# Kernel tuning notes

Measured on AMD Instinct MI355X. Metric: run time of the kernel, lower is better.

## Reference

```python
import jax, jax.numpy as jnp
import numpy as np

N = 8192
DIMS = 128
HID = 64
NEG = -9e15


def setup_inputs() -> dict:
    key = jax.random.key(0)
    k_adj, k_h, k_w1, k_w2 = jax.random.split(key, 4)
    graph_info = (jax.random.uniform(k_adj, (N, N)) < 0.01).astype(jnp.float32)
    h = jax.random.normal(k_h, (N, DIMS), dtype=jnp.float32)
    # xavier-normal-ish init for the 2-layer scoring MLP (dims -> 64 -> 1)
    W1 = jax.random.normal(k_w1, (DIMS, HID), dtype=jnp.float32) * np.sqrt(2.0 / (DIMS + HID))
    b1 = jnp.zeros((HID,), dtype=jnp.float32)
    W2 = jax.random.normal(k_w2, (HID, 1), dtype=jnp.float32) * np.sqrt(2.0 / (HID + 1))
    b2 = jnp.zeros((1,), dtype=jnp.float32)
    return {"graph_info": graph_info, "h": h, "W1": W1, "b1": b1, "W2": W2, "b2": b2}


def reference(graph_info, h, W1, b1, W2, b2):
    # per-node MLP score: e_j for every node j  -> [N, 1]
    e = jnp.dot(jnp.maximum(jnp.dot(h, W1) + b1, 0.0), W2) + b2
    # e.transpose().repeat(N,1): row i sees scores of all columns j -> broadcast [1, N]
    scores = e[:, 0][None, :]
    # mask non-edges with large negative, softmax over neighbors (dim=-1)
    att = jnp.where(graph_info > 0, scores, jnp.float32(NEG))
    att = jax.nn.softmax(att, axis=-1)
    out = jnp.dot(att, h)  # [N, dims] aggregation
    # sum_flag == 1: rescale each row by its degree (diagflat(num) @ h)
    num = jnp.sum(graph_info, axis=-1)  # [N]
    out = num[:, None] * out
    return out
```

## Files before the change

### kernel.cpp

```cpp
#include <hip/hip_runtime.h>
#include <math.h>

#define NN 8192
#define DIMS 128
#define HID 64
#define CAP 192

__global__ __launch_bounds__(256) void score_kernel(
    const float* __restrict__ h, const float* __restrict__ W1,
    const float* __restrict__ b1, const float* __restrict__ W2,
    const float* __restrict__ b2, float* __restrict__ e) {
  int wave = threadIdx.x >> 6;
  int lane = threadIdx.x & 63;
  int j = blockIdx.x * 4 + wave;
  if (j >= NN) return;
  const float* hj = h + (size_t)j * DIMS;
  float acc = b1[lane];
#pragma unroll 8
  for (int d = 0; d < DIMS; ++d) {
    acc = fmaf(hj[d], W1[d * HID + lane], acc);
  }
  float r = fmaxf(acc, 0.0f) * W2[lane];
#pragma unroll
  for (int off = 32; off > 0; off >>= 1) r += __shfl_xor(r, off, 64);
  if (lane == 0) e[j] = r + b2[0];
}

__global__ __launch_bounds__(1024) void expmax_kernel(
    const float* __restrict__ e, float* __restrict__ ee) {
  __shared__ float wmax[16];
  int tid = threadIdx.x;
  float m = -INFINITY;
  for (int i = tid; i < NN; i += 1024) m = fmaxf(m, e[i]);
#pragma unroll
  for (int off = 32; off > 0; off >>= 1) m = fmaxf(m, __shfl_xor(m, off, 64));
  int wave = tid >> 6, lane = tid & 63;
  if (lane == 0) wmax[wave] = m;
  __syncthreads();
  m = wmax[0];
#pragma unroll
  for (int w = 1; w < 16; ++w) m = fmaxf(m, wmax[w]);
  for (int i = tid; i < NN; i += 1024) ee[i] = expf(e[i] - m);
}

__global__ __launch_bounds__(256) void agg_kernel(
    const float* __restrict__ graph, const float* __restrict__ h,
    const float* __restrict__ ee, float* __restrict__ out) {
  __shared__ int   s_idx[4][CAP];
  __shared__ float s_w[4][CAP];
  int w = threadIdx.x >> 6;
  int lane = threadIdx.x & 63;
  int row = blockIdx.x * 4 + w;
  const float4* g4 = (const float4*)(graph + (size_t)row * NN);
  unsigned long long lt = (1ull << lane) - 1ull;
  int cnt = 0;
#pragma unroll 4
  for (int it = 0; it < 32; ++it) {
    float4 v = g4[it * 64 + lane];
    int col = (it * 64 + lane) * 4;
    unsigned long long m0 = __ballot(v.x > 0.f);
    unsigned long long m1 = __ballot(v.y > 0.f);
    unsigned long long m2 = __ballot(v.z > 0.f);
    unsigned long long m3 = __ballot(v.w > 0.f);
    if (v.x > 0.f) { int o = cnt + __popcll(m0 & lt); if (o < CAP) s_idx[w][o] = col; }
    cnt += (int)__popcll(m0);
    if (v.y > 0.f) { int o = cnt + __popcll(m1 & lt); if (o < CAP) s_idx[w][o] = col + 1; }
    cnt += (int)__popcll(m1);
    if (v.z > 0.f) { int o = cnt + __popcll(m2 & lt); if (o < CAP) s_idx[w][o] = col + 2; }
    cnt += (int)__popcll(m2);
    if (v.w > 0.f) { int o = cnt + __popcll(m3 & lt); if (o < CAP) s_idx[w][o] = col + 3; }
    cnt += (int)__popcll(m3);
  }
  int count = cnt < CAP ? cnt : CAP;

  float z = 0.f;
  for (int q = lane; q < count; q += 64) {
    int j = s_idx[w][q];
    float wv = ee[j];
    s_w[w][q] = wv;
    z += wv;
  }
#pragma unroll
  for (int off = 32; off > 0; off >>= 1) z += __shfl_xor(z, off, 64);

  float ax = 0.f, ay = 0.f;
  const float* hbase = h + lane * 2;
#pragma unroll 4
  for (int q = 0; q < count; ++q) {
    int j = s_idx[w][q];
    float wv = s_w[w][q];
    float2 hv = *(const float2*)(hbase + (size_t)j * DIMS);
    ax = fmaf(wv, hv.x, ax);
    ay = fmaf(wv, hv.y, ay);
  }
  float scale = (count > 0) ? ((float)count / z) : 0.f;
  float2 o2 = make_float2(ax * scale, ay * scale);
  *(float2*)(out + (size_t)row * DIMS + lane * 2) = o2;
}

extern "C" void kernel_launch(void* const* d_in, const int* in_sizes, int n_in,
                              void* d_out, int out_size, void* d_ws, size_t ws_size,
                              hipStream_t stream) {
  const float* graph = (const float*)d_in[0];
  const float* h     = (const float*)d_in[1];
  const float* W1    = (const float*)d_in[2];
  const float* b1    = (const float*)d_in[3];
  const float* W2    = (const float*)d_in[4];
  const float* b2    = (const float*)d_in[5];
  float* out = (float*)d_out;
  float* e   = (float*)d_ws;
  float* ee  = e + NN;

  score_kernel<<<NN / 4, 256, 0, stream>>>(h, W1, b1, W2, b2, e);
  expmax_kernel<<<1, 1024, 0, stream>>>(e, ee);
  agg_kernel<<<NN / 4, 256, 0, stream>>>(graph, h, ee, out);
}
```

Measured before the change: 87.00 us.

## Stage W1 in LDS, batch scoring rows, prefetch adjacency with nontemporal loads

The score kernel now stages W1 in shared memory and has each wave compute four nodes at once, launching a quarter as many blocks. The aggregation kernel software-pipelines the adjacency row scan with nontemporal loads, packs weight and index together in LDS, and unrolls the gather by 8 to keep more loads in flight. It also adds an occupancy hint and a nontemporal output store. The aim is to hide memory latency on the dominant 256MB adjacency stream, at the cost of extra registers and 32KB of LDS per score block.

```diff
diff --git a/kernel.cpp b/kernel.cpp
--- a/kernel.cpp
+++ b/kernel.cpp
@@ -6,24 +6,44 @@
 #define HID 64
 #define CAP 192
 
+typedef float f4v __attribute__((ext_vector_type(4)));
+typedef float f2v __attribute__((ext_vector_type(2)));
+
 __global__ __launch_bounds__(256) void score_kernel(
     const float* __restrict__ h, const float* __restrict__ W1,
     const float* __restrict__ b1, const float* __restrict__ W2,
     const float* __restrict__ b2, float* __restrict__ e) {
-  int wave = threadIdx.x >> 6;
-  int lane = threadIdx.x & 63;
-  int j = blockIdx.x * 4 + wave;
-  if (j >= NN) return;
-  const float* hj = h + (size_t)j * DIMS;
-  float acc = b1[lane];
-#pragma unroll 8
+  __shared__ float sW1[DIMS * HID];
+  for (int i = threadIdx.x * 4; i < DIMS * HID; i += 1024)
+    *(float4*)&sW1[i] = *(const float4*)&W1[i];
+  __syncthreads();
+  int wv = threadIdx.x >> 6, lane = threadIdx.x & 63;
+  int j0 = blockIdx.x * 16 + wv * 4;
+  const float* h0 = h + (size_t)j0 * DIMS;
+  float bb = b1[lane];
+  float a0 = bb, a1 = bb, a2 = bb, a3 = bb;
+#pragma unroll 4
   for (int d = 0; d < DIMS; ++d) {
-    acc = fmaf(hj[d], W1[d * HID + lane], acc);
+    float wc = sW1[d * HID + lane];
+    a0 = fmaf(h0[d], wc, a0);
+    a1 = fmaf(h0[d + DIMS], wc, a1);
+    a2 = fmaf(h0[d + 2 * DIMS], wc, a2);
+    a3 = fmaf(h0[d + 3 * DIMS], wc, a3);
   }
-  float r = fmaxf(acc, 0.0f) * W2[lane];
+  float w2 = W2[lane];
+  float r0 = fmaxf(a0, 0.f) * w2, r1 = fmaxf(a1, 0.f) * w2;
+  float r2 = fmaxf(a2, 0.f) * w2, r3 = fmaxf(a3, 0.f) * w2;
 #pragma unroll
-  for (int off = 32; off > 0; off >>= 1) r += __shfl_xor(r, off, 64);
-  if (lane == 0) e[j] = r + b2[0];
+  for (int off = 32; off > 0; off >>= 1) {
+    r0 += __shfl_xor(r0, off, 64);
+    r1 += __shfl_xor(r1, off, 64);
+    r2 += __shfl_xor(r2, off, 64);
+    r3 += __shfl_xor(r3, off, 64);
+  }
+  if (lane == 0) {
+    float bo = b2[0];
+    e[j0] = r0 + bo; e[j0 + 1] = r1 + bo; e[j0 + 2] = r2 + bo; e[j0 + 3] = r3 + bo;
+  }
 }
 
 __global__ __launch_bounds__(1024) void expmax_kernel(
@@ -43,33 +63,58 @@
   for (int i = tid; i < NN; i += 1024) ee[i] = expf(e[i] - m);
 }
 
-__global__ __launch_bounds__(256) void agg_kernel(
+#define PROC(v, it)                                                            \
+  do {                                                                         \
+    int col = ((it) * 64 + lane) * 4;                                          \
+    unsigned long long m0 = __ballot(v.x > 0.f);                               \
+    unsigned long long m1 = __ballot(v.y > 0.f);                               \
+    unsigned long long m2 = __ballot(v.z > 0.f);                               \
+    unsigned long long m3 = __ballot(v.w > 0.f);                               \
+    if (v.x > 0.f) { int o = cnt + __popcll(m0 & lt); if (o < CAP) s_idx[w][o] = col; }     \
+    cnt += (int)__popcll(m0);                                                  \
+    if (v.y > 0.f) { int o = cnt + __popcll(m1 & lt); if (o < CAP) s_idx[w][o] = col + 1; } \
+    cnt += (int)__popcll(m1);                                                  \
+    if (v.z > 0.f) { int o = cnt + __popcll(m2 & lt); if (o < CAP) s_idx[w][o] = col + 2; } \
+    cnt += (int)__popcll(m2);                                                  \
+    if (v.w > 0.f) { int o = cnt + __popcll(m3 & lt); if (o < CAP) s_idx[w][o] = col + 3; } \
+    cnt += (int)__popcll(m3);                                                  \
+  } while (0)
+
+#define HLD(wj) (*(const float2*)(hbase + ((size_t)__float_as_int((wj).y)) * DIMS))
+
+__global__ __launch_bounds__(256, 6) void agg_kernel(
     const float* __restrict__ graph, const float* __restrict__ h,
     const float* __restrict__ ee, float* __restrict__ out) {
-  __shared__ int   s_idx[4][CAP];
-  __shared__ float s_w[4][CAP];
+  __shared__ int s_idx[4][CAP];
+  __shared__ float2 s_wj[4][CAP];
   int w = threadIdx.x >> 6;
   int lane = threadIdx.x & 63;
   int row = blockIdx.x * 4 + w;
-  const float4* g4 = (const float4*)(graph + (size_t)row * NN);
+  const f4v* g4 = (const f4v*)(graph + (size_t)row * NN);
   unsigned long long lt = (1ull << lane) - 1ull;
   int cnt = 0;
-#pragma unroll 4
-  for (int it = 0; it < 32; ++it) {
-    float4 v = g4[it * 64 + lane];
-    int col = (it * 64 + lane) * 4;
-    unsigned long long m0 = __ballot(v.x > 0.f);
-    unsigned long long m1 = __ballot(v.y > 0.f);
-    unsigned long long m2 = __ballot(v.z > 0.f);
-    unsigned long long m3 = __ballot(v.w > 0.f);
-    if (v.x > 0.f) { int o = cnt + __popcll(m0 & lt); if (o < CAP) s_idx[w][o] = col; }
-    cnt += (int)__popcll(m0);
-    if (v.y > 0.f) { int o = cnt + __popcll(m1 & lt); if (o < CAP) s_idx[w][o] = col + 1; }
-    cnt += (int)__popcll(m1);
-    if (v.z > 0.f) { int o = cnt + __popcll(m2 & lt); if (o < CAP) s_idx[w][o] = col + 2; }
-    cnt += (int)__popcll(m2);
-    if (v.w > 0.f) { int o = cnt + __popcll(m3 & lt); if (o < CAP) s_idx[w][o] = col + 3; }
-    cnt += (int)__popcll(m3);
+
+  f4v c0 = __builtin_nontemporal_load(g4 + 0 * 64 + lane);
+  f4v c1 = __builtin_nontemporal_load(g4 + 1 * 64 + lane);
+  f4v c2 = __builtin_nontemporal_load(g4 + 2 * 64 + lane);
+  f4v c3 = __builtin_nontemporal_load(g4 + 3 * 64 + lane);
+#pragma unroll 1
+  for (int it4 = 0; it4 < 8; ++it4) {
+    f4v n0, n1, n2, n3;
+    if (it4 < 7) {
+      const f4v* nb = g4 + (it4 * 4 + 4) * 64 + lane;
+      n0 = __builtin_nontemporal_load(nb);
+      n1 = __builtin_nontemporal_load(nb + 64);
+      n2 = __builtin_nontemporal_load(nb + 128);
+      n3 = __builtin_nontemporal_load(nb + 192);
+    } else {
+      n0 = n1 = n2 = n3 = (f4v)(0.f);
+    }
+    PROC(c0, it4 * 4 + 0);
+    PROC(c1, it4 * 4 + 1);
+    PROC(c2, it4 * 4 + 2);
+    PROC(c3, it4 * 4 + 3);
+    c0 = n0; c1 = n1; c2 = n2; c3 = n3;
   }
   int count = cnt < CAP ? cnt : CAP;
 
@@ -77,7 +122,7 @@
   for (int q = lane; q < count; q += 64) {
     int j = s_idx[w][q];
     float wv = ee[j];
-    s_w[w][q] = wv;
+    s_wj[w][q] = make_float2(wv, __int_as_float(j));
     z += wv;
   }
 #pragma unroll
@@ -85,17 +130,35 @@
 
   float ax = 0.f, ay = 0.f;
   const float* hbase = h + lane * 2;
-#pragma unroll 4
-  for (int q = 0; q < count; ++q) {
-    int j = s_idx[w][q];
-    float wv = s_w[w][q];
-    float2 hv = *(const float2*)(hbase + (size_t)j * DIMS);
-    ax = fmaf(wv, hv.x, ax);
-    ay = fmaf(wv, hv.y, ay);
+  int q = 0;
+  int n8 = count & ~7;
+  for (; q < n8; q += 8) {
+    float2 wj0 = s_wj[w][q + 0], wj1 = s_wj[w][q + 1];
+    float2 wj2 = s_wj[w][q + 2], wj3 = s_wj[w][q + 3];
+    float2 wj4 = s_wj[w][q + 4], wj5 = s_wj[w][q + 5];
+    float2 wj6 = s_wj[w][q + 6], wj7 = s_wj[w][q + 7];
+    float2 h0 = HLD(wj0), h1 = HLD(wj1), h2 = HLD(wj2), h3 = HLD(wj3);
+    float2 h4 = HLD(wj4), h5 = HLD(wj5), h6 = HLD(wj6), h7 = HLD(wj7);
+    ax = fmaf(wj0.x, h0.x, ax); ay = fmaf(wj0.x, h0.y, ay);
+    ax = fmaf(wj1.x, h1.x, ax); ay = fmaf(wj1.x, h1.y, ay);
+    ax = fmaf(wj2.x, h2.x, ax); ay = fmaf(wj2.x, h2.y, ay);
+    ax = fmaf(wj3.x, h3.x, ax); ay = fmaf(wj3.x, h3.y, ay);
+    ax = fmaf(wj4.x, h4.x, ax); ay = fmaf(wj4.x, h4.y, ay);
+    ax = fmaf(wj5.x, h5.x, ax); ay = fmaf(wj5.x, h5.y, ay);
+    ax = fmaf(wj6.x, h6.x, ax); ay = fmaf(wj6.x, h6.y, ay);
+    ax = fmaf(wj7.x, h7.x, ax); ay = fmaf(wj7.x, h7.y, ay);
+  }
+  for (; q < count; ++q) {
+    float2 wj = s_wj[w][q];
+    float2 hv = HLD(wj);
+    ax = fmaf(wj.x, hv.x, ax);
+    ay = fmaf(wj.x, hv.y, ay);
   }
   float scale = (count > 0) ? ((float)count / z) : 0.f;
-  float2 o2 = make_float2(ax * scale, ay * scale);
-  *(float2*)(out + (size_t)row * DIMS + lane * 2) = o2;
+  f2v o2;
+  o2.x = ax * scale;
+  o2.y = ay * scale;
+  __builtin_nontemporal_store(o2, (f2v*)(out + (size_t)row * DIMS + lane * 2));
 }
 
 extern "C" void kernel_launch(void* const* d_in, const int* in_sizes, int n_in,
@@ -111,7 +174,7 @@
   float* e   = (float*)d_ws;
   float* ee  = e + NN;
 
-  score_kernel<<<NN / 4, 256, 0, stream>>>(h, W1, b1, W2, b2, e);
+  score_kernel<<<NN / 16, 256, 0, stream>>>(h, W1, b1, W2, b2, e);
   expmax_kernel<<<1, 1024, 0, stream>>>(e, ee);
   agg_kernel<<<NN / 4, 256, 0, stream>>>(graph, h, ee, out);
 }
```

After: 83.20 us. 4.4% less time.
